# Kernel tuning notes

Hardware: AMD Instinct MI355X
Metric: run time of the kernel (lower is better)

Reference implementation:

```python
import jax, jax.numpy as jnp
import numpy as np

CH = 512
NUM_HEADS = 8
NUM_GROUPS = 32  # min(32, channels)
EPS = 1e-5


def setup_inputs() -> dict:
    key = jax.random.key(0)
    ks = jax.random.split(key, 4)
    B, C, H, W = 8, CH, 32, 32
    x = jax.random.normal(ks[0], (B, C, H, W), dtype=jnp.float32)
    gn_weight = jnp.ones((C,), dtype=jnp.float32)
    gn_bias = jnp.zeros((C,), dtype=jnp.float32)
    # 1x1 conv weights stored as [out_ch, in_ch] (kernel dims squeezed)
    qkv_weight = jax.random.normal(ks[1], (3 * C, C), dtype=jnp.float32) * (C ** -0.5)
    qkv_bias = jnp.zeros((3 * C,), dtype=jnp.float32)
    proj_weight = jax.random.normal(ks[2], (C, C), dtype=jnp.float32) * (C ** -0.5)
    proj_bias = jnp.zeros((C,), dtype=jnp.float32)
    return {
        "x": x,
        "gn_weight": gn_weight,
        "gn_bias": gn_bias,
        "qkv_weight": qkv_weight,
        "qkv_bias": qkv_bias,
        "proj_weight": proj_weight,
        "proj_bias": proj_bias,
    }


def _group_norm(x, weight, bias):
    B, C, H, W = x.shape
    g = x.reshape(B, NUM_GROUPS, C // NUM_GROUPS, H, W)
    mean = jnp.mean(g, axis=(2, 3, 4), keepdims=True)
    var = jnp.var(g, axis=(2, 3, 4), keepdims=True)
    g = (g - mean) * jax.lax.rsqrt(var + EPS)
    g = g.reshape(B, C, H, W)
    return g * weight[None, :, None, None] + bias[None, :, None, None]


def reference(x, gn_weight, gn_bias, qkv_weight, qkv_bias, proj_weight, proj_bias):
    B, C, H, W = x.shape
    nh = NUM_HEADS
    hc = C // nh
    N = H * W

    h = _group_norm(x, gn_weight, gn_bias)
    # 1x1 conv == per-pixel matmul
    qkv = jnp.einsum('oc,bchw->bohw', qkv_weight, h) + qkv_bias[None, :, None, None]
    q, k, v = jnp.split(qkv, 3, axis=1)
    # b (h c) x y -> b h c (x y)
    q = q.reshape(B, nh, hc, N)
    k = k.reshape(B, nh, hc, N)
    v = v.reshape(B, nh, hc, N)

    scale = hc ** -0.5
    attn = jnp.einsum('bhci,bhcj->bhij', q, k) * scale  # [B, nh, N, N]
    attn = jax.nn.softmax(attn, axis=-1)
    out = jnp.einsum('bhij,bhcj->bhci', attn, v)  # [B, nh, hc, N]
    out = out.reshape(B, C, H, W)
    out = jnp.einsum('oc,bchw->bohw', proj_weight, out) + proj_bias[None, :, None, None]
    return x + out
```

## Files before the change

### kernel.cpp

```cpp
#include <hip/hip_runtime.h>
#include <math.h>

#define B_   8
#define C_   512
#define N_   1024
#define NH_  8
#define HC_  64

typedef __attribute__((ext_vector_type(8))) short bf16x8;
typedef __attribute__((ext_vector_type(4))) float f32x4;

#define MFMA16(a, b, c) __builtin_amdgcn_mfma_f32_16x16x32_bf16(a, b, c, 0, 0, 0)

__device__ __forceinline__ unsigned short f2bf(float f) {
  unsigned u = __builtin_bit_cast(unsigned, f);
  u += 0x7fffu + ((u >> 16) & 1u);
  return (unsigned short)(u >> 16);
}

__device__ __forceinline__ void gll16(const void* g, void* l) {
  __builtin_amdgcn_global_load_lds(
      (const __attribute__((address_space(1))) unsigned int*)g,
      (__attribute__((address_space(3))) unsigned int*)l, 16, 0, 0);
}

__global__ __launch_bounds__(256) void wcvt(const float* __restrict__ src,
                                            unsigned short* __restrict__ dst) {
  const int i = (blockIdx.x * 256 + threadIdx.x) * 4;
  const float4 v = *(const float4*)(src + i);
  ushort4 o;
  o.x = f2bf(v.x); o.y = f2bf(v.y); o.z = f2bf(v.z); o.w = f2bf(v.w);
  *(ushort4*)(dst + i) = o;
}

__global__ __launch_bounds__(256) void gn_stats(const float* __restrict__ x,
                                                float* __restrict__ stats) {
  const int b = blockIdx.x >> 5;
  const int g = blockIdx.x & 31;
  const size_t base = ((size_t)b * C_ + (size_t)g * 16) * N_;
  const float4* xp = (const float4*)(x + base);
  float s = 0.f, ss = 0.f;
#pragma unroll
  for (int it = 0; it < 16; ++it) {
    float4 v = xp[it * 256 + threadIdx.x];
    s  += v.x + v.y + v.z + v.w;
    ss += v.x * v.x + v.y * v.y + v.z * v.z + v.w * v.w;
  }
#pragma unroll
  for (int off = 32; off > 0; off >>= 1) {
    s  += __shfl_down(s, off);
    ss += __shfl_down(ss, off);
  }
  __shared__ float rs[4], rss[4];
  if ((threadIdx.x & 63) == 0) { rs[threadIdx.x >> 6] = s; rss[threadIdx.x >> 6] = ss; }
  __syncthreads();
  if (threadIdx.x == 0) {
    s  = rs[0] + rs[1] + rs[2] + rs[3];
    ss = rss[0] + rss[1] + rss[2] + rss[3];
    const float mean = s * (1.f / 16384.f);
    const float var  = ss * (1.f / 16384.f) - mean * mean;
    stats[blockIdx.x * 2]     = mean;
    stats[blockIdx.x * 2 + 1] = rsqrtf(var + 1e-5f);
  }
}

__global__ __launch_bounds__(256) void gn_norm_t(const float* __restrict__ x,
                                                 const float* __restrict__ gw,
                                                 const float* __restrict__ gb,
                                                 const float* __restrict__ stats,
                                                 unsigned short* __restrict__ hT) {
  __shared__ __attribute__((aligned(16))) unsigned short Lt[64][72];
  const int t = threadIdx.x;
  const int p0 = blockIdx.x * 64, c0 = blockIdx.y * 64, b = blockIdx.z;
#pragma unroll
  for (int u = 0; u < 4; ++u) {
    const int idx = u * 256 + t;
    const int cc = idx >> 4, p4 = idx & 15;
    const int c = c0 + cc;
    const int sidx = (b * 32 + (c >> 4)) * 2;
    const float mean = stats[sidx], inv = stats[sidx + 1];
    const float sc = inv * gw[c];
    const float of = gb[c] - mean * sc;
    const float4 v = *(const float4*)&x[((size_t)(b * C_ + c)) * N_ + p0 + p4 * 4];
    Lt[p4 * 4 + 0][cc] = f2bf(v.x * sc + of);
    Lt[p4 * 4 + 1][cc] = f2bf(v.y * sc + of);
    Lt[p4 * 4 + 2][cc] = f2bf(v.z * sc + of);
    Lt[p4 * 4 + 3][cc] = f2bf(v.w * sc + of);
  }
  __syncthreads();
#pragma unroll
  for (int u = 0; u < 2; ++u) {
    const int idx = u * 256 + t;
    const int p = idx >> 3, oc = idx & 7;
    *(uint4*)&hT[((size_t)(b * N_) + p0 + p) * C_ + c0 + oc * 8] =
        *(const uint4*)&Lt[p][oc * 8];
  }
}

template <int MODE>
__global__ __launch_bounds__(256, 2) void gemm_bt(
    const unsigned short* __restrict__ A, const float* __restrict__ bias,
    const unsigned short* __restrict__ BT, const float* __restrict__ resid,
    float* __restrict__ outf, unsigned short* __restrict__ qkTout,
    unsigned short* __restrict__ vout) {
  __shared__ __attribute__((aligned(16))) short lds[16 * 512];
  const int t = threadIdx.x;
  const int lane = t & 63, w = t >> 6;
  const int lm = lane & 15, q = lane >> 4;
  const int wm = w >> 1, wn = w & 1;
  const int b = blockIdx.z;
  const int m0 = blockIdx.y * 128, n0 = blockIdx.x * 128;
  const unsigned short* Bb = BT + (size_t)b * N_ * C_;

  f32x4 acc[4][4];
#pragma unroll
  for (int i = 0; i < 4; ++i)
#pragma unroll
    for (int j = 0; j < 4; ++j) acc[i][j] = (f32x4){0.f, 0.f, 0.f, 0.f};

  for (int k0 = 0; k0 < C_; k0 += 32) {
    __syncthreads();
#pragma unroll
    for (int ff = 0; ff < 2; ++ff) {
      const int f = w * 2 + ff;
      gll16(A  + (size_t)(m0 + f * 16 + lm) * C_ + k0 + q * 8, lds + f * 512);
      gll16(Bb + (size_t)(n0 + f * 16 + lm) * C_ + k0 + q * 8, lds + (8 + f) * 512);
    }
    __syncthreads();
    bf16x8 af[4], bf[4];
#pragma unroll
    for (int mi = 0; mi < 4; ++mi)
      af[mi] = *(const bf16x8*)(lds + (wm * 4 + mi) * 512 + lane * 8);
#pragma unroll
    for (int ni = 0; ni < 4; ++ni)
      bf[ni] = *(const bf16x8*)(lds + (8 + wn * 4 + ni) * 512 + lane * 8);
#pragma unroll
    for (int mi = 0; mi < 4; ++mi)
#pragma unroll
      for (int ni = 0; ni < 4; ++ni)
        acc[mi][ni] = MFMA16(af[mi], bf[ni], acc[mi][ni]);
  }

  if (MODE == 0) {
    if (blockIdx.y < 8) {
      const bool isQ = (blockIdx.y < 4);
#pragma unroll
      for (int mi = 0; mi < 4; ++mi) {
#pragma unroll
        for (int ni = 0; ni < 4; ++ni) {
          const int col  = n0 + wn * 64 + ni * 16 + lm;
          const int row0 = m0 + wm * 64 + mi * 16 + q * 4;
          ushort4 o4;
          float v0 = acc[mi][ni][0] + bias[row0 + 0];
          float v1 = acc[mi][ni][1] + bias[row0 + 1];
          float v2 = acc[mi][ni][2] + bias[row0 + 2];
          float v3 = acc[mi][ni][3] + bias[row0 + 3];
          if (isQ) { v0 *= 0.125f; v1 *= 0.125f; v2 *= 0.125f; v3 *= 0.125f; }
          o4.x = f2bf(v0); o4.y = f2bf(v1); o4.z = f2bf(v2); o4.w = f2bf(v3);
          *(ushort4*)&qkTout[((size_t)b * N_ + col) * 1024 + row0] = o4;
        }
      }
    } else {
#pragma unroll
      for (int mi = 0; mi < 4; ++mi)
#pragma unroll
        for (int ni = 0; ni < 4; ++ni) {
          const int col = n0 + wn * 64 + ni * 16 + lm;
#pragma unroll
          for (int r = 0; r < 4; ++r) {
            const int row = m0 + wm * 64 + mi * 16 + q * 4 + r;
            vout[((size_t)b * 512 + row - 1024) * N_ + col] =
                f2bf(acc[mi][ni][r] + bias[row]);
          }
        }
    }
  } else {
#pragma unroll
    for (int mi = 0; mi < 4; ++mi)
#pragma unroll
      for (int ni = 0; ni < 4; ++ni) {
        const int col = n0 + wn * 64 + ni * 16 + lm;
#pragma unroll
        for (int r = 0; r < 4; ++r) {
          const int row = m0 + wm * 64 + mi * 16 + q * 4 + r;
          const size_t oi = ((size_t)b * 512 + row) * N_ + col;
          outf[oi] = acc[mi][ni][r] + bias[row] + resid[oi];
        }
      }
  }
}

__global__ __launch_bounds__(256, 2) void attn_mfma(
    const unsigned short* __restrict__ qkT, const unsigned short* __restrict__ vbuf,
    unsigned short* __restrict__ aoT) {
  __shared__ __attribute__((aligned(16))) short lds[48 * 512];
  short* Qb = lds;
  short* Kb = lds + 16 * 512;
  short* Vb = lds + 24 * 512;
  short* Pb = lds + 32 * 512;

  const int t = threadIdx.x;
  const int lane = t & 63, w = t >> 6;
  const int lm = lane & 15, q = lane >> 4;
  const int i0 = blockIdx.x * 128;
  const int hh = blockIdx.y;
  const int b = blockIdx.z;

  const unsigned short* QT = qkT + (size_t)b * N_ * 1024;
  const unsigned short* Vp = vbuf + ((size_t)b * 512 + hh * 64) * N_;

#pragma unroll
  for (int ff = 0; ff < 4; ++ff) {
    const int f = w * 4 + ff;
    gll16(QT + (size_t)(i0 + (f >> 1) * 16 + lm) * 1024 + hh * 64 + (f & 1) * 32 + q * 8,
          Qb + f * 512);
  }
  __syncthreads();

  bf16x8 af[2][2];
#pragma unroll
  for (int mi = 0; mi < 2; ++mi)
#pragma unroll
    for (int ks = 0; ks < 2; ++ks)
      af[mi][ks] = *(const bf16x8*)(Qb + ((w * 2 + mi) * 2 + ks) * 512 + lane * 8);

  f32x4 accO[2][4], lrun[2];
#pragma unroll
  for (int mi = 0; mi < 2; ++mi) {
    lrun[mi] = (f32x4){0.f, 0.f, 0.f, 0.f};
#pragma unroll
    for (int nc = 0; nc < 4; ++nc) accO[mi][nc] = (f32x4){0.f, 0.f, 0.f, 0.f};
  }

  for (int jt = 0; jt < 16; ++jt) {
    const int j0 = jt * 64;
    __syncthreads();
#pragma unroll
    for (int ks = 0; ks < 2; ++ks) {
      const int f = w * 2 + ks;
      gll16(QT + (size_t)(j0 + w * 16 + lm) * 1024 + 512 + hh * 64 + ks * 32 + q * 8,
            Kb + f * 512);
      gll16(Vp + (size_t)(w * 16 + lm) * N_ + j0 + ks * 32 + q * 8, Vb + f * 512);
    }
    __syncthreads();

    f32x4 accS[2][4];
#pragma unroll
    for (int mi = 0; mi < 2; ++mi)
#pragma unroll
      for (int nj = 0; nj < 4; ++nj) accS[mi][nj] = (f32x4){0.f, 0.f, 0.f, 0.f};
#pragma unroll
    for (int nj = 0; nj < 4; ++nj)
#pragma unroll
      for (int ks = 0; ks < 2; ++ks) {
        const bf16x8 bfr = *(const bf16x8*)(Kb + (nj * 2 + ks) * 512 + lane * 8);
#pragma unroll
        for (int mi = 0; mi < 2; ++mi)
          accS[mi][nj] = MFMA16(af[mi][ks], bfr, accS[mi][nj]);
      }

#pragma unroll
    for (int mi = 0; mi < 2; ++mi) {
#pragma unroll
      for (int nj = 0; nj < 4; ++nj)
#pragma unroll
        for (int r = 0; r < 4; ++r) {
          const float p = __expf(accS[mi][nj][r]);
          accS[mi][nj][r] = p;
          lrun[mi][r] += p;
        }
#pragma unroll
      for (int nj = 0; nj < 4; ++nj) {
        const int jin = nj * 16 + lm;
        const int ks = jin >> 5;
        const int qt = (jin >> 3) & 3;
        const int jp = jin & 7;
        short* pp = Pb + (w * 4 + mi * 2 + ks) * 512 + qt * 128 + jp;
#pragma unroll
        for (int r = 0; r < 4; ++r)
          pp[(q * 4 + r) * 8] = (short)f2bf(accS[mi][nj][r]);
      }
    }

#pragma unroll
    for (int ks = 0; ks < 2; ++ks) {
      bf16x8 pf[2];
#pragma unroll
      for (int mi = 0; mi < 2; ++mi)
        pf[mi] = *(const bf16x8*)(Pb + (w * 4 + mi * 2 + ks) * 512 + lane * 8);
#pragma unroll
      for (int nc = 0; nc < 4; ++nc) {
        const bf16x8 vf = *(const bf16x8*)(Vb + (nc * 2 + ks) * 512 + lane * 8);
#pragma unroll
        for (int mi = 0; mi < 2; ++mi)
          accO[mi][nc] = MFMA16(pf[mi], vf, accO[mi][nc]);
      }
    }
  }

  unsigned short* aob = aoT + (size_t)b * N_ * C_;
#pragma unroll
  for (int mi = 0; mi < 2; ++mi) {
#pragma unroll
    for (int d = 1; d <= 8; d <<= 1)
#pragma unroll
      for (int r = 0; r < 4; ++r) lrun[mi][r] += __shfl_xor(lrun[mi][r], d);
    f32x4 linv;
#pragma unroll
    for (int r = 0; r < 4; ++r) linv[r] = 1.f / lrun[mi][r];
#pragma unroll
    for (int nc = 0; nc < 4; ++nc) {
      const int col = hh * 64 + nc * 16 + lm;
#pragma unroll
      for (int r = 0; r < 4; ++r) {
        const int i = i0 + w * 32 + mi * 16 + q * 4 + r;
        aob[(size_t)i * C_ + col] = f2bf(accO[mi][nc][r] * linv[r]);
      }
    }
  }
}

extern "C" void kernel_launch(void* const* d_in, const int* in_sizes, int n_in,
                              void* d_out, int out_size, void* d_ws, size_t ws_size,
                              hipStream_t stream) {
  const float* x    = (const float*)d_in[0];
  const float* gw   = (const float*)d_in[1];
  const float* gb   = (const float*)d_in[2];
  const float* qkvw = (const float*)d_in[3];
  const float* qkvb = (const float*)d_in[4];
  const float* pw   = (const float*)d_in[5];
  const float* pb   = (const float*)d_in[6];
  float* out = (float*)d_out;

  unsigned short* hT       = (unsigned short*)d_ws;
  unsigned short* qkvw_bf  = hT + (size_t)B_ * N_ * C_;
  unsigned short* projw_bf = qkvw_bf + 1536 * 512;
  unsigned short* qkT      = projw_bf + 512 * 512;
  unsigned short* vbuf     = qkT + (size_t)B_ * N_ * 1024;
  unsigned short* aoTp     = vbuf + (size_t)B_ * 512 * N_;
  float* stats             = (float*)(aoTp + (size_t)B_ * N_ * C_);

  wcvt<<<768, 256, 0, stream>>>(qkvw, qkvw_bf);
  wcvt<<<256, 256, 0, stream>>>(pw, projw_bf);
  gn_stats<<<256, 256, 0, stream>>>(x, stats);
  gn_norm_t<<<dim3(16, 8, B_), 256, 0, stream>>>(x, gw, gb, stats, hT);
  gemm_bt<0><<<dim3(8, 12, B_), 256, 0, stream>>>(qkvw_bf, qkvb, hT, nullptr,
                                                  nullptr, qkT, vbuf);
  attn_mfma<<<dim3(8, NH_, B_), 256, 0, stream>>>(qkT, vbuf, aoTp);
  gemm_bt<1><<<dim3(8, 4, B_), 256, 0, stream>>>(projw_bf, pb, aoTp, x, out,
                                                 nullptr, nullptr);
}
```

Baseline: 175.6 us.

## Fuse prep kernels and shrink attention and proj tiles for more blocks

Merges the weight conversion, group-norm statistics and normalize-transpose into a single prep kernel that keeps each group's data in registers, so x is read once and four launches become one. The attention kernel now gives each block 64 query rows instead of 128, with smaller LDS use and a higher occupancy hint, doubling the grid. The projection GEMM gets its own kernel with 128x64 tiles, doubling its grid, and the QKV GEMM's occupancy hint is raised. The trade-offs are more redundant K/V loads per query row in attention, higher register pressure in prep, and only 256 blocks doing the group-norm work.

```diff
diff --git a/kernel.cpp b/kernel.cpp
--- a/kernel.cpp
+++ b/kernel.cpp
@@ -18,90 +18,98 @@
   return (unsigned short)(u >> 16);
 }
 
+__device__ __forceinline__ unsigned pack2(float a, float b) {
+  return (unsigned)f2bf(a) | ((unsigned)f2bf(b) << 16);
+}
+
 __device__ __forceinline__ void gll16(const void* g, void* l) {
   __builtin_amdgcn_global_load_lds(
       (const __attribute__((address_space(1))) unsigned int*)g,
       (__attribute__((address_space(3))) unsigned int*)l, 16, 0, 0);
 }
 
-__global__ __launch_bounds__(256) void wcvt(const float* __restrict__ src,
-                                            unsigned short* __restrict__ dst) {
-  const int i = (blockIdx.x * 256 + threadIdx.x) * 4;
-  const float4 v = *(const float4*)(src + i);
-  ushort4 o;
-  o.x = f2bf(v.x); o.y = f2bf(v.y); o.z = f2bf(v.z); o.w = f2bf(v.w);
-  *(ushort4*)(dst + i) = o;
-}
-
-__global__ __launch_bounds__(256) void gn_stats(const float* __restrict__ x,
-                                                float* __restrict__ stats) {
+__global__ __launch_bounds__(256) void prep(const float* __restrict__ x,
+                                            const float* __restrict__ gw,
+                                            const float* __restrict__ gb,
+                                            const float* __restrict__ qkvw,
+                                            const float* __restrict__ pw,
+                                            unsigned short* __restrict__ hT,
+                                            unsigned short* __restrict__ qkvw_bf,
+                                            unsigned short* __restrict__ projw_bf) {
+  const int t = threadIdx.x;
+  if (blockIdx.x >= 256) {
+    const int widx = blockIdx.x - 256;
+    const float* src = (widx < 768) ? qkvw : pw;
+    unsigned short* dst = (widx < 768) ? qkvw_bf : projw_bf;
+    const int i = ((widx < 768) ? widx : widx - 768) * 1024 + t * 4;
+    const float4 v = *(const float4*)(src + i);
+    ushort4 o;
+    o.x = f2bf(v.x); o.y = f2bf(v.y); o.z = f2bf(v.z); o.w = f2bf(v.w);
+    *(ushort4*)(dst + i) = o;
+    return;
+  }
   const int b = blockIdx.x >> 5;
   const int g = blockIdx.x & 31;
-  const size_t base = ((size_t)b * C_ + (size_t)g * 16) * N_;
-  const float4* xp = (const float4*)(x + base);
+  const float* xg = x + ((size_t)b * C_ + (size_t)g * 16) * N_;
+
+  float4 xv[16];
   float s = 0.f, ss = 0.f;
 #pragma unroll
-  for (int it = 0; it < 16; ++it) {
-    float4 v = xp[it * 256 + threadIdx.x];
-    s  += v.x + v.y + v.z + v.w;
-    ss += v.x * v.x + v.y * v.y + v.z * v.z + v.w * v.w;
+  for (int k = 0; k < 16; ++k) {
+    xv[k] = *(const float4*)(xg + (size_t)k * N_ + t * 4);
+    s  += xv[k].x + xv[k].y + xv[k].z + xv[k].w;
+    ss += xv[k].x * xv[k].x + xv[k].y * xv[k].y + xv[k].z * xv[k].z + xv[k].w * xv[k].w;
   }
 #pragma unroll
   for (int off = 32; off > 0; off >>= 1) {
     s  += __shfl_down(s, off);
     ss += __shfl_down(ss, off);
   }
-  __shared__ float rs[4], rss[4];
-  if ((threadIdx.x & 63) == 0) { rs[threadIdx.x >> 6] = s; rss[threadIdx.x >> 6] = ss; }
+  __shared__ float rs[4], rss[4], sh_mi[2];
+  if ((t & 63) == 0) { rs[t >> 6] = s; rss[t >> 6] = ss; }
   __syncthreads();
-  if (threadIdx.x == 0) {
+  if (t == 0) {
     s  = rs[0] + rs[1] + rs[2] + rs[3];
     ss = rss[0] + rss[1] + rss[2] + rss[3];
     const float mean = s * (1.f / 16384.f);
     const float var  = ss * (1.f / 16384.f) - mean * mean;
-    stats[blockIdx.x * 2]     = mean;
-    stats[blockIdx.x * 2 + 1] = rsqrtf(var + 1e-5f);
-  }
-}
-
-__global__ __launch_bounds__(256) void gn_norm_t(const float* __restrict__ x,
-                                                 const float* __restrict__ gw,
-                                                 const float* __restrict__ gb,
-                                                 const float* __restrict__ stats,
-                                                 unsigned short* __restrict__ hT) {
-  __shared__ __attribute__((aligned(16))) unsigned short Lt[64][72];
-  const int t = threadIdx.x;
-  const int p0 = blockIdx.x * 64, c0 = blockIdx.y * 64, b = blockIdx.z;
-#pragma unroll
-  for (int u = 0; u < 4; ++u) {
-    const int idx = u * 256 + t;
-    const int cc = idx >> 4, p4 = idx & 15;
-    const int c = c0 + cc;
-    const int sidx = (b * 32 + (c >> 4)) * 2;
-    const float mean = stats[sidx], inv = stats[sidx + 1];
-    const float sc = inv * gw[c];
-    const float of = gb[c] - mean * sc;
-    const float4 v = *(const float4*)&x[((size_t)(b * C_ + c)) * N_ + p0 + p4 * 4];
-    Lt[p4 * 4 + 0][cc] = f2bf(v.x * sc + of);
-    Lt[p4 * 4 + 1][cc] = f2bf(v.y * sc + of);
-    Lt[p4 * 4 + 2][cc] = f2bf(v.z * sc + of);
-    Lt[p4 * 4 + 3][cc] = f2bf(v.w * sc + of);
+    sh_mi[0] = mean;
+    sh_mi[1] = rsqrtf(var + 1e-5f);
   }
   __syncthreads();
-#pragma unroll
-  for (int u = 0; u < 2; ++u) {
-    const int idx = u * 256 + t;
-    const int p = idx >> 3, oc = idx & 7;
-    *(uint4*)&hT[((size_t)(b * N_) + p0 + p) * C_ + c0 + oc * 8] =
-        *(const uint4*)&Lt[p][oc * 8];
-  }
-}
-
-template <int MODE>
-__global__ __launch_bounds__(256, 2) void gemm_bt(
+  const float mean = sh_mi[0], inv = sh_mi[1];
+
+  float sc[16], of[16];
+#pragma unroll
+  for (int k = 0; k < 16; ++k) {
+    const int c = g * 16 + k;
+    sc[k] = inv * gw[c];
+    of[k] = gb[c] - mean * sc[k];
+  }
+#pragma unroll
+  for (int r = 0; r < 4; ++r) {
+    const int p = t * 4 + r;
+    unsigned short* dst = hT + ((size_t)b * N_ + p) * C_ + g * 16;
+    uint4 o0, o1;
+    const float* f0 = (const float*)&xv[0];
+#pragma unroll
+    for (int k2 = 0; k2 < 4; ++k2) {
+      const float a0 = ((const float*)&xv[k2 * 2 + 0])[r] * sc[k2 * 2 + 0] + of[k2 * 2 + 0];
+      const float a1 = ((const float*)&xv[k2 * 2 + 1])[r] * sc[k2 * 2 + 1] + of[k2 * 2 + 1];
+      ((unsigned*)&o0)[k2] = pack2(a0, a1);
+      const float b0 = ((const float*)&xv[8 + k2 * 2 + 0])[r] * sc[8 + k2 * 2 + 0] + of[8 + k2 * 2 + 0];
+      const float b1 = ((const float*)&xv[8 + k2 * 2 + 1])[r] * sc[8 + k2 * 2 + 1] + of[8 + k2 * 2 + 1];
+      ((unsigned*)&o1)[k2] = pack2(b0, b1);
+    }
+    (void)f0;
+    *(uint4*)(dst)     = o0;
+    *(uint4*)(dst + 8) = o1;
+  }
+}
+
+__global__ __launch_bounds__(256, 3) void gemm_qkv(
     const unsigned short* __restrict__ A, const float* __restrict__ bias,
-    const unsigned short* __restrict__ BT, const float* __restrict__ resid,
-    float* __restrict__ outf, unsigned short* __restrict__ qkTout,
+    const unsigned short* __restrict__ BT, unsigned short* __restrict__ qkTout,
     unsigned short* __restrict__ vout) {
   __shared__ __attribute__((aligned(16))) short lds[16 * 512];
   const int t = threadIdx.x;
@@ -141,38 +149,23 @@
         acc[mi][ni] = MFMA16(af[mi], bf[ni], acc[mi][ni]);
   }
 
-  if (MODE == 0) {
-    if (blockIdx.y < 8) {
-      const bool isQ = (blockIdx.y < 4);
-#pragma unroll
-      for (int mi = 0; mi < 4; ++mi) {
-#pragma unroll
-        for (int ni = 0; ni < 4; ++ni) {
-          const int col  = n0 + wn * 64 + ni * 16 + lm;
-          const int row0 = m0 + wm * 64 + mi * 16 + q * 4;
-          ushort4 o4;
-          float v0 = acc[mi][ni][0] + bias[row0 + 0];
-          float v1 = acc[mi][ni][1] + bias[row0 + 1];
-          float v2 = acc[mi][ni][2] + bias[row0 + 2];
-          float v3 = acc[mi][ni][3] + bias[row0 + 3];
-          if (isQ) { v0 *= 0.125f; v1 *= 0.125f; v2 *= 0.125f; v3 *= 0.125f; }
-          o4.x = f2bf(v0); o4.y = f2bf(v1); o4.z = f2bf(v2); o4.w = f2bf(v3);
-          *(ushort4*)&qkTout[((size_t)b * N_ + col) * 1024 + row0] = o4;
-        }
-      }
-    } else {
-#pragma unroll
-      for (int mi = 0; mi < 4; ++mi)
-#pragma unroll
-        for (int ni = 0; ni < 4; ++ni) {
-          const int col = n0 + wn * 64 + ni * 16 + lm;
-#pragma unroll
-          for (int r = 0; r < 4; ++r) {
-            const int row = m0 + wm * 64 + mi * 16 + q * 4 + r;
-            vout[((size_t)b * 512 + row - 1024) * N_ + col] =
-                f2bf(acc[mi][ni][r] + bias[row]);
-          }
-        }
+  if (blockIdx.y < 8) {
+    const bool isQ = (blockIdx.y < 4);
+#pragma unroll
+    for (int mi = 0; mi < 4; ++mi) {
+#pragma unroll
+      for (int ni = 0; ni < 4; ++ni) {
+        const int col  = n0 + wn * 64 + ni * 16 + lm;
+        const int row0 = m0 + wm * 64 + mi * 16 + q * 4;
+        float v0 = acc[mi][ni][0] + bias[row0 + 0];
+        float v1 = acc[mi][ni][1] + bias[row0 + 1];
+        float v2 = acc[mi][ni][2] + bias[row0 + 2];
+        float v3 = acc[mi][ni][3] + bias[row0 + 3];
+        if (isQ) { v0 *= 0.125f; v1 *= 0.125f; v2 *= 0.125f; v3 *= 0.125f; }
+        ushort4 o4;
+        o4.x = f2bf(v0); o4.y = f2bf(v1); o4.z = f2bf(v2); o4.w = f2bf(v3);
+        *(ushort4*)&qkTout[((size_t)b * N_ + col) * 1024 + row0] = o4;
+      }
     }
   } else {
 #pragma unroll
@@ -183,26 +176,82 @@
 #pragma unroll
         for (int r = 0; r < 4; ++r) {
           const int row = m0 + wm * 64 + mi * 16 + q * 4 + r;
-          const size_t oi = ((size_t)b * 512 + row) * N_ + col;
-          outf[oi] = acc[mi][ni][r] + bias[row] + resid[oi];
+          vout[((size_t)b * 512 + row - 1024) * N_ + col] =
+              f2bf(acc[mi][ni][r] + bias[row]);
         }
       }
   }
 }
 
-__global__ __launch_bounds__(256, 2) void attn_mfma(
-    const unsigned short* __restrict__ qkT, const unsigned short* __restrict__ vbuf,
-    unsigned short* __restrict__ aoT) {
-  __shared__ __attribute__((aligned(16))) short lds[48 * 512];
-  short* Qb = lds;
-  short* Kb = lds + 16 * 512;
-  short* Vb = lds + 24 * 512;
-  short* Pb = lds + 32 * 512;
-
+__global__ __launch_bounds__(256, 2) void gemm_proj(
+    const unsigned short* __restrict__ A, const float* __restrict__ bias,
+    const unsigned short* __restrict__ BT, const float* __restrict__ resid,
+    float* __restrict__ outf) {
+  __shared__ __attribute__((aligned(16))) short lds[12 * 512];
   const int t = threadIdx.x;
   const int lane = t & 63, w = t >> 6;
   const int lm = lane & 15, q = lane >> 4;
-  const int i0 = blockIdx.x * 128;
+  const int wm = w >> 1, wn = w & 1;
+  const int b = blockIdx.z;
+  const int m0 = blockIdx.y * 128, n0 = blockIdx.x * 64;
+  const unsigned short* Bb = BT + (size_t)b * N_ * C_;
+
+  f32x4 acc[4][2];
+#pragma unroll
+  for (int i = 0; i < 4; ++i)
+#pragma unroll
+    for (int j = 0; j < 2; ++j) acc[i][j] = (f32x4){0.f, 0.f, 0.f, 0.f};
+
+  for (int k0 = 0; k0 < C_; k0 += 32) {
+    __syncthreads();
+#pragma unroll
+    for (int ff = 0; ff < 2; ++ff) {
+      const int f = w * 2 + ff;
+      gll16(A + (size_t)(m0 + f * 16 + lm) * C_ + k0 + q * 8, lds + f * 512);
+    }
+    gll16(Bb + (size_t)(n0 + w * 16 + lm) * C_ + k0 + q * 8, lds + (8 + w) * 512);
+    __syncthreads();
+    bf16x8 af[4], bf[2];
+#pragma unroll
+    for (int mi = 0; mi < 4; ++mi)
+      af[mi] = *(const bf16x8*)(lds + (wm * 4 + mi) * 512 + lane * 8);
+#pragma unroll
+    for (int ni = 0; ni < 2; ++ni)
+      bf[ni] = *(const bf16x8*)(lds + (8 + wn * 2 + ni) * 512 + lane * 8);
+#pragma unroll
+    for (int mi = 0; mi < 4; ++mi)
+#pragma unroll
+      for (int ni = 0; ni < 2; ++ni)
+        acc[mi][ni] = MFMA16(af[mi], bf[ni], acc[mi][ni]);
+  }
+
+#pragma unroll
+  for (int mi = 0; mi < 4; ++mi)
+#pragma unroll
+    for (int ni = 0; ni < 2; ++ni) {
+      const int col = n0 + wn * 32 + ni * 16 + lm;
+#pragma unroll
+      for (int r = 0; r < 4; ++r) {
+        const int row = m0 + wm * 64 + mi * 16 + q * 4 + r;
+        const size_t oi = ((size_t)b * 512 + row) * N_ + col;
+        outf[oi] = acc[mi][ni][r] + bias[row] + resid[oi];
+      }
+    }
+}
+
+__global__ __launch_bounds__(256, 4) void attn_mfma(
+    const unsigned short* __restrict__ qkT, const unsigned short* __restrict__ vbuf,
+    unsigned short* __restrict__ aoT) {
+  __shared__ __attribute__((aligned(16))) short lds[32 * 512];
+  short* Qb = lds;
+  short* Kb = lds + 8 * 512;
+  short* Vb = lds + 16 * 512;
+  short* Pb = lds + 24 * 512;
+
+  const int t = threadIdx.x;
+  const int lane = t & 63, w = t >> 6;
+  const int lm = lane & 15, q = lane >> 4;
+  const int i0 = blockIdx.x * 64;
   const int hh = blockIdx.y;
   const int b = blockIdx.z;
 
@@ -210,112 +259,90 @@
   const unsigned short* Vp = vbuf + ((size_t)b * 512 + hh * 64) * N_;
 
 #pragma unroll
-  for (int ff = 0; ff < 4; ++ff) {
-    const int f = w * 4 + ff;
-    gll16(QT + (size_t)(i0 + (f >> 1) * 16 + lm) * 1024 + hh * 64 + (f & 1) * 32 + q * 8,
-          Qb + f * 512);
-  }
+  for (int ff = 0; ff < 2; ++ff)
+    gll16(QT + (size_t)(i0 + w * 16 + lm) * 1024 + hh * 64 + ff * 32 + q * 8,
+          Qb + (w * 2 + ff) * 512);
   __syncthreads();
 
-  bf16x8 af[2][2];
-#pragma unroll
-  for (int mi = 0; mi < 2; ++mi)
-#pragma unroll
-    for (int ks = 0; ks < 2; ++ks)
-      af[mi][ks] = *(const bf16x8*)(Qb + ((w * 2 + mi) * 2 + ks) * 512 + lane * 8);
-
-  f32x4 accO[2][4], lrun[2];
-#pragma unroll
-  for (int mi = 0; mi < 2; ++mi) {
-    lrun[mi] = (f32x4){0.f, 0.f, 0.f, 0.f};
-#pragma unroll
-    for (int nc = 0; nc < 4; ++nc) accO[mi][nc] = (f32x4){0.f, 0.f, 0.f, 0.f};
-  }
+  bf16x8 af[2];
+#pragma unroll
+  for (int ks = 0; ks < 2; ++ks)
+    af[ks] = *(const bf16x8*)(Qb + (w * 2 + ks) * 512 + lane * 8);
+
+  f32x4 accO[4], lrun = (f32x4){0.f, 0.f, 0.f, 0.f};
+#pragma unroll
+  for (int nc = 0; nc < 4; ++nc) accO[nc] = (f32x4){0.f, 0.f, 0.f, 0.f};
 
   for (int jt = 0; jt < 16; ++jt) {
     const int j0 = jt * 64;
     __syncthreads();
 #pragma unroll
     for (int ks = 0; ks < 2; ++ks) {
-      const int f = w * 2 + ks;
       gll16(QT + (size_t)(j0 + w * 16 + lm) * 1024 + 512 + hh * 64 + ks * 32 + q * 8,
-            Kb + f * 512);
-      gll16(Vp + (size_t)(w * 16 + lm) * N_ + j0 + ks * 32 + q * 8, Vb + f * 512);
-    }
-    __syncthreads();
-
-    f32x4 accS[2][4];
-#pragma unroll
-    for (int mi = 0; mi < 2; ++mi)
-#pragma unroll
-      for (int nj = 0; nj < 4; ++nj) accS[mi][nj] = (f32x4){0.f, 0.f, 0.f, 0.f};
+            Kb + (w * 2 + ks) * 512);
+      gll16(Vp + (size_t)(w * 16 + lm) * N_ + j0 + ks * 32 + q * 8,
+            Vb + (w * 2 + ks) * 512);
+    }
+    __syncthreads();
+
+    f32x4 accS[4];
+#pragma unroll
+    for (int nj = 0; nj < 4; ++nj) accS[nj] = (f32x4){0.f, 0.f, 0.f, 0.f};
 #pragma unroll
     for (int nj = 0; nj < 4; ++nj)
 #pragma unroll
       for (int ks = 0; ks < 2; ++ks) {
         const bf16x8 bfr = *(const bf16x8*)(Kb + (nj * 2 + ks) * 512 + lane * 8);
-#pragma unroll
-        for (int mi = 0; mi < 2; ++mi)
-          accS[mi][nj] = MFMA16(af[mi][ks], bfr, accS[mi][nj]);
-      }
-
-#pragma unroll
-    for (int mi = 0; mi < 2; ++mi) {
-#pragma unroll
-      for (int nj = 0; nj < 4; ++nj)
-#pragma unroll
-        for (int r = 0; r < 4; ++r) {
-          const float p = __expf(accS[mi][nj][r]);
-          accS[mi][nj][r] = p;
-          lrun[mi][r] += p;
-        }
-#pragma unroll
-      for (int nj = 0; nj < 4; ++nj) {
-        const int jin = nj * 16 + lm;
-        const int ks = jin >> 5;
-        const int qt = (jin >> 3) & 3;
-        const int jp = jin & 7;
-        short* pp = Pb + (w * 4 + mi * 2 + ks) * 512 + qt * 128 + jp;
-#pragma unroll
-        for (int r = 0; r < 4; ++r)
-          pp[(q * 4 + r) * 8] = (short)f2bf(accS[mi][nj][r]);
-      }
+        accS[nj] = MFMA16(af[ks], bfr, accS[nj]);
+      }
+
+#pragma unroll
+    for (int nj = 0; nj < 4; ++nj)
+#pragma unroll
+      for (int r = 0; r < 4; ++r) {
+        const float p = __expf(accS[nj][r]);
+        accS[nj][r] = p;
+        lrun[r] += p;
+      }
+#pragma unroll
+    for (int nj = 0; nj < 4; ++nj) {
+      const int jin = nj * 16 + lm;
+      const int ks = jin >> 5;
+      const int qt = (jin >> 3) & 3;
+      const int jp = jin & 7;
+      short* pp = Pb + (w * 2 + ks) * 512 + qt * 128 + jp;
+#pragma unroll
+      for (int r = 0; r < 4; ++r)
+        pp[(q * 4 + r) * 8] = (short)f2bf(accS[nj][r]);
     }
 
 #pragma unroll
     for (int ks = 0; ks < 2; ++ks) {
-      bf16x8 pf[2];
-#pragma unroll
-      for (int mi = 0; mi < 2; ++mi)
-        pf[mi] = *(const bf16x8*)(Pb + (w * 4 + mi * 2 + ks) * 512 + lane * 8);
+      const bf16x8 pf = *(const bf16x8*)(Pb + (w * 2 + ks) * 512 + lane * 8);
 #pragma unroll
       for (int nc = 0; nc < 4; ++nc) {
         const bf16x8 vf = *(const bf16x8*)(Vb + (nc * 2 + ks) * 512 + lane * 8);
-#pragma unroll
-        for (int mi = 0; mi < 2; ++mi)
-          accO[mi][nc] = MFMA16(pf[mi], vf, accO[mi][nc]);
-      }
-    }
-  }
+        accO[nc] = MFMA16(pf, vf, accO[nc]);
+      }
+    }
+  }
+
+#pragma unroll
+  for (int d = 1; d <= 8; d <<= 1)
+#pragma unroll
+    for (int r = 0; r < 4; ++r) lrun[r] += __shfl_xor(lrun[r], d);
+  f32x4 linv;
+#pragma unroll
+  for (int r = 0; r < 4; ++r) linv[r] = 1.f / lrun[r];
 
   unsigned short* aob = aoT + (size_t)b * N_ * C_;
 #pragma unroll
-  for (int mi = 0; mi < 2; ++mi) {
-#pragma unroll
-    for (int d = 1; d <= 8; d <<= 1)
-#pragma unroll
-      for (int r = 0; r < 4; ++r) lrun[mi][r] += __shfl_xor(lrun[mi][r], d);
-    f32x4 linv;
-#pragma unroll
-    for (int r = 0; r < 4; ++r) linv[r] = 1.f / lrun[mi][r];
-#pragma unroll
-    for (int nc = 0; nc < 4; ++nc) {
-      const int col = hh * 64 + nc * 16 + lm;
-#pragma unroll
-      for (int r = 0; r < 4; ++r) {
-        const int i = i0 + w * 32 + mi * 16 + q * 4 + r;
-        aob[(size_t)i * C_ + col] = f2bf(accO[mi][nc][r] * linv[r]);
-      }
+  for (int nc = 0; nc < 4; ++nc) {
+    const int col = hh * 64 + nc * 16 + lm;
+#pragma unroll
+    for (int r = 0; r < 4; ++r) {
+      const int i = i0 + w * 16 + q * 4 + r;
+      aob[(size_t)i * C_ + col] = f2bf(accO[nc][r] * linv[r]);
     }
   }
 }
@@ -338,15 +365,9 @@
   unsigned short* qkT      = projw_bf + 512 * 512;
   unsigned short* vbuf     = qkT + (size_t)B_ * N_ * 1024;
   unsigned short* aoTp     = vbuf + (size_t)B_ * 512 * N_;
-  float* stats             = (float*)(aoTp + (size_t)B_ * N_ * C_);
-
-  wcvt<<<768, 256, 0, stream>>>(qkvw, qkvw_bf);
-  wcvt<<<256, 256, 0, stream>>>(pw, projw_bf);
-  gn_stats<<<256, 256, 0, stream>>>(x, stats);
-  gn_norm_t<<<dim3(16, 8, B_), 256, 0, stream>>>(x, gw, gb, stats, hT);
-  gemm_bt<0><<<dim3(8, 12, B_), 256, 0, stream>>>(qkvw_bf, qkvb, hT, nullptr,
-                                                  nullptr, qkT, vbuf);
-  attn_mfma<<<dim3(8, NH_, B_), 256, 0, stream>>>(qkT, vbuf, aoTp);
-  gemm_bt<1><<<dim3(8, 4, B_), 256, 0, stream>>>(projw_bf, pb, aoTp, x, out,
-                                                 nullptr, nullptr);
-}
+
+  prep<<<1280, 256, 0, stream>>>(x, gw, gb, qkvw, pw, hT, qkvw_bf, projw_bf);
+  gemm_qkv<<<dim3(8, 12, B_), 256, 0, stream>>>(qkvw_bf, qkvb, hT, qkT, vbuf);
+  attn_mfma<<<dim3(16, NH_, B_), 256, 0, stream>>>(qkT, vbuf, aoTp);
+  gemm_proj<<<dim3(16, 4, B_), 256, 0, stream>>>(projw_bf, pb, aoTp, x, out);
+}
```

Result: faster. 166.9 us (-4.9%).
